# Kernel tuning notes

Hardware: AMD Instinct MI355X
Metric: run time of the kernel (lower is better)

Reference implementation:

```python
import jax, jax.numpy as jnp
import numpy as np

N_NODES = 100000
N_EDGES = 1_600_000
D = 32


def setup_inputs() -> dict:
    key = jax.random.key(0)
    k1, k2, k3, k4, k5 = jax.random.split(key, 5)
    x = jax.random.normal(k1, (N_NODES, D), dtype=jnp.float32)
    W1 = jax.random.normal(k2, (D, D), dtype=jnp.float32) * (1.0 / np.sqrt(D))
    W2 = jax.random.normal(k3, (D, D), dtype=jnp.float32) * (1.0 / np.sqrt(D))
    b2 = jax.random.normal(k4, (D,), dtype=jnp.float32) * 0.01
    edge_index = jax.random.randint(k5, (2, N_EDGES), 0, N_NODES, dtype=jnp.int64)
    return {"x": x, "W1": W1, "W2": W2, "b2": b2, "edge_index": edge_index}


def reference(x, W1, W2, b2, edge_index):
    # ptensors0.transfer0 over the graph: F1[i] = sum_{(j->i) in E} x[j]
    src = edge_index[0]
    dst = edge_index[1]
    F1 = jax.ops.segment_sum(x[src], dst, num_segments=x.shape[0])  # [N, D]
    # out = lin2(x) + lin1(F1)  (lin2 has bias, lin1 does not; torch Linear: y = x @ W.T + b)
    return x @ W2.T + b2 + F1 @ W1.T
```

## Files before the change

kernel.cpp:

```cpp
#include <hip/hip_runtime.h>
#include <hip/hip_bf16.h>

#define DIM 32
#define LOG_NPB 7
#define NPB 128
#define CAP 4096
#define NBINS 800
#define EPB 12288
#define EPT 12

__global__ __launch_bounds__(256) void fused_lin_kernel(
    const float* __restrict__ x,
    const float* __restrict__ W1,
    const float* __restrict__ W2,
    const float* __restrict__ b2,
    float* __restrict__ out,
    unsigned* __restrict__ y32,
    int* __restrict__ cursor, int nb,
    int n_nodes)
{
    __shared__ float W1s[DIM][DIM];
    __shared__ float W2s[DIM][DIM];
    __shared__ float b2s[DIM];
    __shared__ float xs[8][DIM];

    const int t = threadIdx.x;

    if (blockIdx.x == 0) {
        for (int i = t; i < nb; i += 256) cursor[i] = i * CAP;
    }

    for (int i = t; i < DIM * DIM; i += 256) {
        int c = i >> 5, k = i & 31;
        W1s[k][c] = W1[i];
        W2s[k][c] = W2[i];
    }
    if (t < DIM) b2s[t] = b2[t];

    const int r = t >> 5;
    const int c = t & 31;
    const int ntiles = (n_nodes + 7) >> 3;

    for (int tile = blockIdx.x; tile < ntiles; tile += gridDim.x) {
        const int row = tile * 8 + r;
        __syncthreads();
        if (row < n_nodes) xs[r][c] = x[(long)row * DIM + c];
        __syncthreads();
        if (row < n_nodes) {
            float a2 = b2s[c];
            float a1 = 0.0f;
            #pragma unroll
            for (int k = 0; k < DIM; ++k) {
                float xv = xs[r][k];
                a2 += xv * W2s[k][c];
                a1 += xv * W1s[k][c];
            }
            out[(long)row * DIM + c] = a2;
            float hi = __shfl_down(a1, 1);
            if ((c & 1) == 0) {
                __hip_bfloat16 blo = __float2bfloat16(a1);
                __hip_bfloat16 bhi = __float2bfloat16(hi);
                unsigned pack = ((unsigned)(*(unsigned short*)&bhi) << 16)
                              | (unsigned)(*(unsigned short*)&blo);
                y32[(size_t)row * 16 + (c >> 1)] = pack;
            }
        }
    }
}

__global__ __launch_bounds__(1024) void bucket_scatter_kernel(
    const int* __restrict__ src, const int* __restrict__ dst,
    int* __restrict__ cursor, unsigned* __restrict__ bedges, int nE)
{
    __shared__ unsigned stage[EPB];
    __shared__ int cnt[NBINS];
    __shared__ int ex[NBINS];
    __shared__ int gbase[NBINS];
    __shared__ int scanbuf[1024];

    const int t = threadIdx.x;
    const long blockStart = (long)blockIdx.x * EPB;

    for (int i = t; i < NBINS; i += 1024) cnt[i] = 0;
    __syncthreads();

    #pragma unroll
    for (int i = 0; i < EPT; ++i) {
        long e = blockStart + (long)i * 1024 + t;
        if (e < nE) atomicAdd(&cnt[dst[e] >> LOG_NPB], 1);
    }
    __syncthreads();

    int v = (t < NBINS) ? cnt[t] : 0;
    scanbuf[t] = v;
    __syncthreads();
    for (int off = 1; off < 1024; off <<= 1) {
        int add = (t >= off) ? scanbuf[t - off] : 0;
        __syncthreads();
        scanbuf[t] += add;
        __syncthreads();
    }
    if (t < NBINS) ex[t] = scanbuf[t] - v;
    __syncthreads();

    for (int b = t; b < NBINS; b += 1024) {
        int c = cnt[b];
        if (c > 0) gbase[b] = atomicAdd(&cursor[b], c);
    }
    scanbuf[t] = 0;
    __syncthreads();

    #pragma unroll
    for (int i = 0; i < EPT; ++i) {
        long e = blockStart + (long)i * 1024 + t;
        if (e < nE) {
            int es = src[e];
            int ed = dst[e];
            int b  = ed >> LOG_NPB;
            int r  = atomicAdd(&scanbuf[b], 1);
            stage[ex[b] + r] = ((unsigned)es << LOG_NPB) | (unsigned)(ed & (NPB - 1));
        }
    }
    __syncthreads();

    const int wv   = t >> 6;
    const int lane = t & 63;
    for (int b = wv; b < NBINS; b += 16) {
        int c = cnt[b];
        if (c == 0) continue;
        int lbase = ex[b];
        int gb    = gbase[b];
        int cmax  = (b + 1) * CAP - gb;
        if (cmax < 0) cmax = 0;
        if (c > cmax) c = cmax;
        for (int j = lane; j < c; j += 64)
            bedges[gb + j] = stage[lbase + j];
    }
}

__global__ __launch_bounds__(512) void sort_gather_kernel(
    const int* __restrict__ cursor, const unsigned* __restrict__ bedges,
    const unsigned short* __restrict__ yb,
    float* __restrict__ out, int n_nodes)
{
    __shared__ unsigned ent[CAP];
    __shared__ unsigned sorted[CAP];
    __shared__ int cnt[NPB];
    __shared__ int ex[NPB];
    __shared__ int cur[NPB];

    const int b = blockIdx.x;
    const int t = threadIdx.x;
    const int start = b * CAP;
    int n = cursor[b] - start;
    if (n > CAP) n = CAP;
    if (n < 0) n = 0;

    if (t < NPB) { cnt[t] = 0; cur[t] = 0; }
    __syncthreads();

    for (int i = t; i < n; i += 512) {
        unsigned e = bedges[start + i];
        ent[i] = e;
        atomicAdd(&cnt[e & (NPB - 1)], 1);
    }
    __syncthreads();

    if (t < NPB) ex[t] = cnt[t];
    __syncthreads();
    for (int off = 1; off < NPB; off <<= 1) {
        int add = 0;
        if (t < NPB && t >= off) add = ex[t - off];
        __syncthreads();
        if (t < NPB) ex[t] += add;
        __syncthreads();
    }
    if (t < NPB) ex[t] -= cnt[t];
    __syncthreads();

    for (int i = t; i < n; i += 512) {
        unsigned e = ent[i];
        int bin = (int)(e & (NPB - 1));
        int r = atomicAdd(&cur[bin], 1);
        sorted[ex[bin] + r] = e >> LOG_NPB;
    }
    __syncthreads();

    const int wv   = t >> 6;
    const int lane = t & 63;
    const int slot = lane >> 3;
    const int li   = lane & 7;

    int ln   = wv;
    int node = b * NPB + ln;
    if (node >= n_nodes) return;

    int st = ex[ln];
    int d  = cnt[ln];
    int s[4];
    #pragma unroll
    for (int k = 0; k < 4; ++k) {
        int e = slot + 8 * k;
        int idx = (e < d) ? e : (d > 0 ? d - 1 : 0);
        s[k] = (int)sorted[(d > 0 ? st : 0) + idx];
    }
    float4 o = make_float4(0.f, 0.f, 0.f, 0.f);
    if (slot == 0) o = ((const float4*)(out + ((size_t)node << 5)))[li];

    while (true) {
        ushort4 u[4];
        #pragma unroll
        for (int k = 0; k < 4; ++k) {
            if (8 * k < d)
                u[k] = *(const ushort4*)(yb + ((size_t)s[k] << 5) + (li << 2));
        }

        const int ln_n   = ln + 8;
        const int node_n = node + 8;
        const bool have_n = (ln_n < NPB) && (node_n < n_nodes);
        int st_n = 0, d_n = 0;
        int sn[4];
        float4 o_n = make_float4(0.f, 0.f, 0.f, 0.f);
        if (have_n) {
            st_n = ex[ln_n];
            d_n  = cnt[ln_n];
            #pragma unroll
            for (int k = 0; k < 4; ++k) {
                int e = slot + 8 * k;
                int idx = (e < d_n) ? e : (d_n > 0 ? d_n - 1 : 0);
                sn[k] = (int)sorted[(d_n > 0 ? st_n : 0) + idx];
            }
            if (slot == 0) o_n = ((const float4*)(out + ((size_t)node_n << 5)))[li];
        }

        float a0 = 0.f, a1 = 0.f, a2 = 0.f, a3 = 0.f;
        #pragma unroll
        for (int k = 0; k < 4; ++k) {
            if (8 * k < d) {
                const bool v = (slot + 8 * k) < d;
                a0 += v ? __uint_as_float((unsigned)u[k].x << 16) : 0.f;
                a1 += v ? __uint_as_float((unsigned)u[k].y << 16) : 0.f;
                a2 += v ? __uint_as_float((unsigned)u[k].z << 16) : 0.f;
                a3 += v ? __uint_as_float((unsigned)u[k].w << 16) : 0.f;
            }
        }
        for (int e0 = 32 + slot; e0 < d; e0 += 8) {
            int ss = (int)sorted[st + e0];
            ushort4 uu = *(const ushort4*)(yb + ((size_t)ss << 5) + (li << 2));
            a0 += __uint_as_float((unsigned)uu.x << 16);
            a1 += __uint_as_float((unsigned)uu.y << 16);
            a2 += __uint_as_float((unsigned)uu.z << 16);
            a3 += __uint_as_float((unsigned)uu.w << 16);
        }

        #pragma unroll
        for (int m = 8; m < 64; m <<= 1) {
            a0 += __shfl_xor(a0, m);
            a1 += __shfl_xor(a1, m);
            a2 += __shfl_xor(a2, m);
            a3 += __shfl_xor(a3, m);
        }

        if (slot == 0 && d > 0) {
            float4 w;
            w.x = o.x + a0; w.y = o.y + a1; w.z = o.z + a2; w.w = o.w + a3;
            ((float4*)(out + ((size_t)node << 5)))[li] = w;
        }

        if (!have_n) break;
        ln = ln_n; node = node_n; st = st_n; d = d_n;
        s[0] = sn[0]; s[1] = sn[1]; s[2] = sn[2]; s[3] = sn[3];
        o = o_n;
    }
}

extern "C" void kernel_launch(void* const* d_in, const int* in_sizes, int n_in,
                              void* d_out, int out_size, void* d_ws, size_t ws_size,
                              hipStream_t stream) {
    const float* x  = (const float*)d_in[0];
    const float* W1 = (const float*)d_in[1];
    const float* W2 = (const float*)d_in[2];
    const float* b2 = (const float*)d_in[3];
    const int*   ei = (const int*)d_in[4];

    const int n_nodes = in_sizes[0] / DIM;
    const int n_edges = in_sizes[4] / 2;
    const int* src = ei;
    const int* dst = ei + n_edges;
    float* out = (float*)d_out;

    const int nb = (n_nodes + NPB - 1) / NPB;

    char* basep = (char*)d_ws;
    size_t off = 0;
    auto alloc = [&](size_t bytes) {
        char* p = basep + off;
        off = (off + bytes + 255) & ~(size_t)255;
        return p;
    };
    unsigned* y32    = (unsigned*)alloc((size_t)n_nodes * DIM * sizeof(unsigned short));
    int*      cursor = (int*)     alloc((size_t)nb * sizeof(int));
    unsigned* bedges = (unsigned*)alloc((size_t)nb * CAP * sizeof(unsigned));
    (void)ws_size;

    fused_lin_kernel<<<1024, 256, 0, stream>>>(x, W1, W2, b2, out, y32, cursor, nb, n_nodes);
    bucket_scatter_kernel<<<(n_edges + EPB - 1) / EPB, 1024, 0, stream>>>(src, dst, cursor, bedges, n_edges);
    sort_gather_kernel<<<nb, 512, 0, stream>>>(cursor, bedges, (const unsigned short*)y32, out, n_nodes);
}
```

Before: 89.12 us.

## Single-pass bucket scatter with register-held ranks and smaller per-block tiles

Shrinks the edges per block from 12288 to 4096, giving about 3x more blocks. The scatter now loads src/dst once, keeps each edge's bin, packed value and shared-atomic rank in registers, and drops the second global read pass and second atomic pass. The copy-out loop now uses 16-lane groups per bin instead of full 64-lane waves, since each block holds far fewer edges per bin. In exchange there are more global cursor atomics and more per-block prefix scans.

```diff
diff --git a/kernel.cpp b/kernel.cpp
--- a/kernel.cpp
+++ b/kernel.cpp
@@ -6,8 +6,8 @@
 #define NPB 128
 #define CAP 4096
 #define NBINS 800
-#define EPB 12288
-#define EPT 12
+#define EPB 4096
+#define EPT 4
 
 __global__ __launch_bounds__(256) void fused_lin_kernel(
     const float* __restrict__ x,
@@ -84,57 +84,55 @@
     for (int i = t; i < NBINS; i += 1024) cnt[i] = 0;
     __syncthreads();
 
-    #pragma unroll
-    for (int i = 0; i < EPT; ++i) {
-        long e = blockStart + (long)i * 1024 + t;
-        if (e < nE) atomicAdd(&cnt[dst[e] >> LOG_NPB], 1);
-    }
-    __syncthreads();
-
-    int v = (t < NBINS) ? cnt[t] : 0;
-    scanbuf[t] = v;
-    __syncthreads();
-    for (int off = 1; off < 1024; off <<= 1) {
-        int add = (t >= off) ? scanbuf[t - off] : 0;
-        __syncthreads();
-        scanbuf[t] += add;
-        __syncthreads();
-    }
-    if (t < NBINS) ex[t] = scanbuf[t] - v;
-    __syncthreads();
-
-    for (int b = t; b < NBINS; b += 1024) {
-        int c = cnt[b];
-        if (c > 0) gbase[b] = atomicAdd(&cursor[b], c);
-    }
-    scanbuf[t] = 0;
-    __syncthreads();
-
+    int bn[EPT], rk[EPT];
+    unsigned pk[EPT];
     #pragma unroll
     for (int i = 0; i < EPT; ++i) {
         long e = blockStart + (long)i * 1024 + t;
         if (e < nE) {
-            int es = src[e];
-            int ed = dst[e];
-            int b  = ed >> LOG_NPB;
-            int r  = atomicAdd(&scanbuf[b], 1);
-            stage[ex[b] + r] = ((unsigned)es << LOG_NPB) | (unsigned)(ed & (NPB - 1));
-        }
-    }
-    __syncthreads();
-
-    const int wv   = t >> 6;
-    const int lane = t & 63;
-    for (int b = wv; b < NBINS; b += 16) {
+            int s  = src[e];
+            int dd = dst[e];
+            bn[i] = dd >> LOG_NPB;
+            pk[i] = ((unsigned)s << LOG_NPB) | (unsigned)(dd & (NPB - 1));
+            rk[i] = atomicAdd(&cnt[bn[i]], 1);
+        } else bn[i] = -1;
+    }
+    __syncthreads();
+
+    for (int b = t; b < NBINS; b += 1024) {
+        int c = cnt[b];
+        if (c > 0) gbase[b] = atomicAdd(&cursor[b], c);
+    }
+
+    int v = (t < NBINS) ? cnt[t] : 0;
+    scanbuf[t] = v;
+    __syncthreads();
+    for (int off = 1; off < 1024; off <<= 1) {
+        int add = (t >= off) ? scanbuf[t - off] : 0;
+        __syncthreads();
+        scanbuf[t] += add;
+        __syncthreads();
+    }
+    if (t < NBINS) ex[t] = scanbuf[t] - v;
+    __syncthreads();
+
+    #pragma unroll
+    for (int i = 0; i < EPT; ++i)
+        if (bn[i] >= 0) stage[ex[bn[i]] + rk[i]] = pk[i];
+    __syncthreads();
+
+    const int g   = t >> 4;
+    const int l16 = t & 15;
+    for (int b = g; b < NBINS; b += 64) {
         int c = cnt[b];
         if (c == 0) continue;
-        int lbase = ex[b];
-        int gb    = gbase[b];
-        int cmax  = (b + 1) * CAP - gb;
+        int lb = ex[b];
+        int gb = gbase[b];
+        int cmax = (b + 1) * CAP - gb;
         if (cmax < 0) cmax = 0;
         if (c > cmax) c = cmax;
-        for (int j = lane; j < c; j += 64)
-            bedges[gb + j] = stage[lbase + j];
+        for (int j = l16; j < c; j += 16)
+            bedges[gb + j] = stage[lb + j];
     }
 }
 
```

Result: faster. 82.21 us (-7.8%).
